# Kernel optimization log

Measured on AMD Instinct MI355X. Metric: run time of the kernel, lower is better.

The kernel has to match this reference:

```python
import jax, jax.numpy as jnp
import numpy as np

CUTOFFS = [2000, 10000, 50000]
HIDDEN = 1024
BATCH = 2048


def setup_inputs() -> dict:
    key = jax.random.key(0)
    ks = jax.random.split(key, 8)
    s = 1.0 / np.sqrt(HIDDEN)
    return {
        "hidden": jax.random.normal(ks[0], (BATCH, HIDDEN), dtype=jnp.float32),
        "target": jax.random.randint(ks[1], (BATCH,), 0, CUTOFFS[-1]),
        # head weight: candidates[:cutoffs[0]] plus 2 tail vectors, transposed -> (hidden, 2002)
        "head_w": jax.random.normal(ks[2], (HIDDEN, CUTOFFS[0] + 2), dtype=jnp.float32) * s,
        # tail 0 (cluster [2000,10000), size 8000): down 1024->1024 (rf^0), decode 1024->8000
        "down0": jax.random.normal(ks[3], (HIDDEN, HIDDEN), dtype=jnp.float32) * s,
        "dec0": jax.random.normal(ks[4], (HIDDEN, CUTOFFS[1] - CUTOFFS[0]), dtype=jnp.float32) * s,
        # tail 1 (cluster [10000,50000), size 40000): down 1024->256 (rf^1), decode 256->40000
        "down1": jax.random.normal(ks[5], (HIDDEN, HIDDEN // 4), dtype=jnp.float32) * s,
        "dec1": jax.random.normal(ks[6], (HIDDEN // 4, CUTOFFS[2] - CUTOFFS[1]), dtype=jnp.float32) * s,
    }


def reference(hidden, target, head_w, down0, dec0, down1, dec1):
    # Head logits over first bucket + one pseudo-token per tail cluster.
    head = hidden @ head_w  # (B, 2002)
    # Cluster membership masks (fixed shapes instead of data-dependent gather;
    # rows outside a cluster produce zeroed logits, matching index_select semantics
    # up to padding).
    m0 = ((target >= CUTOFFS[0]) & (target < CUTOFFS[1])).astype(hidden.dtype)
    m1 = ((target >= CUTOFFS[1]) & (target < CUTOFFS[2])).astype(hidden.dtype)
    # Grouped small matmuls: down-project then decode per tail cluster.
    t0 = ((hidden @ down0) @ dec0) * m0[:, None]  # (B, 8000)
    t1 = ((hidden @ down1) @ dec1) * m1[:, None]  # (B, 40000)
    return jnp.concatenate([head, t0, t1], axis=1)  # (B, 50002)
```

## Files before the change

kernel.cpp:

```cpp
#include <hip/hip_runtime.h>

typedef unsigned short u16;
typedef unsigned int   u32;
typedef __attribute__((ext_vector_type(4))) float  f32x4;
typedef __attribute__((ext_vector_type(8))) __bf16 bf16x8;
typedef __attribute__((ext_vector_type(8))) u16    u16x8;
typedef __attribute__((address_space(1))) void as1_void;
typedef __attribute__((address_space(3))) void as3_void;

__device__ int g_idx0[2048];
__device__ int g_idx1[2048];
__device__ int g_cnt[2];

__device__ __forceinline__ void async16(const void* g, void* l) {
  __builtin_amdgcn_global_load_lds((const as1_void*)g, (as3_void*)l, 16, 0, 0);
}

__device__ __forceinline__ u16 f2bf(float f) {
  u32 u = __builtin_bit_cast(u32, f);
  return (u16)((u + 0x7fffu + ((u >> 16) & 1u)) >> 16);
}

template <int MODE>
__device__ __forceinline__ void gemm_core(
    u16* As, u16* Bs,
    const u16* __restrict__ A, const u16* __restrict__ Bt,
    void* __restrict__ Cout, int K, int ldc, int colOff, int Nreal,
    const int* __restrict__ idx, int cnt, int bm, int bn)
{
  const int tid  = threadIdx.x;
  const int wid  = tid >> 6;
  const int lane = tid & 63;
  const int quad = lane >> 4;
  const int l16  = lane & 15;
  const int wm = (wid >> 1) * 64;
  const int wn = (wid & 1) * 64;

  f32x4 acc[4][4] = {};

  const int srow = wid * 16 + (lane >> 2);
  const int scol = (lane & 3) * 8;

  size_t ar0, ar1;
  if (MODE == 1) { ar0 = (size_t)idx[bm + srow]; ar1 = (size_t)idx[bm + srow + 64]; }
  else           { ar0 = (size_t)(bm + srow);    ar1 = ar0 + 64; }
  const u16* ga0 = A + ar0 * K + scol;
  const u16* ga1 = A + ar1 * K + scol;
  const u16* gb0 = Bt + (size_t)(bn + srow) * K + scol;
  const u16* gb1 = gb0 + (size_t)64 * K;

  for (int k0 = 0; k0 < K; k0 += 32) {
    async16(ga0 + k0, As + wid * 512);
    async16(ga1 + k0, As + wid * 512 + 2048);
    async16(gb0 + k0, Bs + wid * 512);
    async16(gb1 + k0, Bs + wid * 512 + 2048);
    __syncthreads();

    bf16x8 af[4], bfr[4];
#pragma unroll
    for (int i = 0; i < 4; i++) {
      af[i]  = *reinterpret_cast<const bf16x8*>(As + (wm + i * 16 + l16) * 32 + quad * 8);
      bfr[i] = *reinterpret_cast<const bf16x8*>(Bs + (wn + i * 16 + l16) * 32 + quad * 8);
    }
#pragma unroll
    for (int mi = 0; mi < 4; mi++)
#pragma unroll
      for (int ni = 0; ni < 4; ni++)
        acc[mi][ni] = __builtin_amdgcn_mfma_f32_16x16x32_bf16(af[mi], bfr[ni], acc[mi][ni], 0, 0, 0);
    __syncthreads();
  }

#pragma unroll
  for (int mi = 0; mi < 4; mi++) {
    const int rbase = bm + wm + mi * 16 + quad * 4;
    int  orow[4];
    bool vld[4];
#pragma unroll
    for (int r = 0; r < 4; r++) {
      if (MODE == 2) {
        int slot = rbase + r;
        vld[r]  = slot < cnt;
        orow[r] = vld[r] ? idx[slot] : 0;
      } else {
        vld[r] = true; orow[r] = rbase + r;
      }
    }
#pragma unroll
    for (int ni = 0; ni < 4; ni++) {
      const int col = bn + wn + ni * 16 + l16;
      if (MODE == 1) {
        u16* C = (u16*)Cout;
#pragma unroll
        for (int r = 0; r < 4; r++)
          C[(size_t)orow[r] * ldc + col] = f2bf(acc[mi][ni][r]);
      } else {
        if (col < Nreal) {
          float* C = (float*)Cout;
#pragma unroll
          for (int r = 0; r < 4; r++)
            if (vld[r]) C[(size_t)orow[r] * ldc + colOff + col] = acc[mi][ni][r];
        }
      }
    }
  }
}

__device__ __forceinline__ void tconv_core(float (*tile)[33], const float* __restrict__ in,
                                           u16* __restrict__ out, int K, int N, int bx, int by) {
  int tx = threadIdx.x & 31, ty = threadIdx.x >> 5;
  int n0 = bx * 32, k0 = by * 32;
#pragma unroll
  for (int i = 0; i < 4; i++) {
    int k = k0 + ty + i * 8;
    int n = n0 + tx;
    tile[ty + i * 8][tx] = (n < N) ? in[(size_t)k * N + n] : 0.0f;
  }
  __syncthreads();
#pragma unroll
  for (int i = 0; i < 4; i++)
    out[(size_t)(n0 + ty + i * 8) * K + k0 + tx] = f2bf(tile[tx][ty + i * 8]);
}

__global__ __launch_bounds__(256) void prep(
    const float* __restrict__ hidden, const int* __restrict__ target,
    const float* __restrict__ head_w, const float* __restrict__ down0,
    const float* __restrict__ dec0, const float* __restrict__ down1,
    const float* __restrict__ dec1,
    u16* __restrict__ hA, u16* __restrict__ head_wT, u16* __restrict__ down0T,
    u16* __restrict__ dec0T, u16* __restrict__ down1T, u16* __restrict__ dec1T)
{
  __shared__ float tile[32][33];
  __shared__ int cc[2];
  const int b = blockIdx.x;
  const int tid = threadIdx.x;
  if (b < 1024) {
    int i = b * 256 + tid;
    const float4* p = reinterpret_cast<const float4*>(hidden) + (size_t)i * 2;
    float4 a = p[0], c = p[1];
    u16x8 o;
    o[0] = f2bf(a.x); o[1] = f2bf(a.y); o[2] = f2bf(a.z); o[3] = f2bf(a.w);
    o[4] = f2bf(c.x); o[5] = f2bf(c.y); o[6] = f2bf(c.z); o[7] = f2bf(c.w);
    reinterpret_cast<u16x8*>(hA)[i] = o;
  } else if (b < 3072) {
    int r = b - 1024;  tconv_core(tile, head_w, head_wT, 1024, 2002,  r % 64,   r / 64);
  } else if (b < 4096) {
    int r = b - 3072;  tconv_core(tile, down0,  down0T,  1024, 1024,  r % 32,   r / 32);
  } else if (b < 12160) {
    int r = b - 4096;  tconv_core(tile, dec0,   dec0T,   1024, 8000,  r % 252,  r / 252);
  } else if (b < 12416) {
    int r = b - 12160; tconv_core(tile, down1,  down1T,  1024, 256,   r % 8,    r / 8);
  } else if (b < 22432) {
    int r = b - 12416; tconv_core(tile, dec1,   dec1T,   256,  40000, r % 1252, r / 1252);
  } else {
    if (tid < 2) cc[tid] = 0;
    __syncthreads();
    for (int i = tid; i < 2048; i += 256) {
      int t = target[i];
      if (t >= 2000 && t < 10000)  g_idx0[atomicAdd(&cc[0], 1)] = i;
      else if (t >= 10000)         g_idx1[atomicAdd(&cc[1], 1)] = i;
    }
    __syncthreads();
    int n0 = cc[0], n1 = cc[1];
    for (int i = tid; i < 2048; i += 256) {
      if (i >= n0) g_idx0[i] = 0;
      if (i >= n1) g_idx1[i] = 0;
    }
    if (tid == 0) { g_cnt[0] = n0; g_cnt[1] = n1; }
  }
}

__global__ __launch_bounds__(256, 2) void g1(
    const u16* __restrict__ hA, const u16* __restrict__ head_wT,
    const u16* __restrict__ down0T, const u16* __restrict__ down1T,
    u16* __restrict__ X0c, u16* __restrict__ X1c, float* __restrict__ out)
{
  __shared__ u16 As[4096], Bs[4096];
  const int b = blockIdx.x;
  if (b < 256) {
    gemm_core<0>(As, Bs, hA, head_wT, out, 1024, 50002, 0, 2002,
                 nullptr, 2048, (b >> 4) * 128, (b & 15) * 128);
  } else if (b < 384) {
    int r = b - 256, bm = (r & 15) * 128, bn = (r >> 4) * 128;
    if (bm < g_cnt[0])
      gemm_core<1>(As, Bs, hA, down0T, X0c, 1024, 1024, 0, 1024, g_idx0, g_cnt[0], bm, bn);
  } else {
    int r = b - 384, bm = (r & 15) * 128, bn = (r >> 4) * 128;
    if (bm < g_cnt[1])
      gemm_core<1>(As, Bs, hA, down1T, X1c, 1024, 256, 0, 256, g_idx1, g_cnt[1], bm, bn);
  }
}

__global__ __launch_bounds__(256, 2) void g2(
    const u16* __restrict__ X0c, const u16* __restrict__ X1c,
    const u16* __restrict__ dec0T, const u16* __restrict__ dec1T,
    const int* __restrict__ target, float* __restrict__ out)
{
  __shared__ u16 As[4096], Bs[4096];
  const int b = blockIdx.x;
  if (b < 1008) {
    int bm = (b & 15) * 128, bn = (b >> 4) * 128;
    if (bm < g_cnt[0])
      gemm_core<2>(As, Bs, X0c, dec0T, out, 1024, 50002, 2002, 8000, g_idx0, g_cnt[0], bm, bn);
  } else if (b < 6016) {
    int r = b - 1008, bm = (r & 15) * 128, bn = (r >> 4) * 128;
    if (bm < g_cnt[1])
      gemm_core<2>(As, Bs, X1c, dec1T, out, 256, 50002, 10002, 40000, g_idx1, g_cnt[1], bm, bn);
  } else {
    int row = b - 6016;
    int t = target[row];
    bool in0 = (t >= 2000) && (t < 10000);
    bool in1 = (t >= 10000);
    float2* p = reinterpret_cast<float2*>(out + (size_t)row * 50002);
    float2 z; z.x = 0.0f; z.y = 0.0f;
    if (!in0)
      for (int i = threadIdx.x; i < 4000; i += 256)  p[1001 + i] = z;
    if (!in1)
      for (int i = threadIdx.x; i < 20000; i += 256) p[5001 + i] = z;
  }
}

extern "C" void kernel_launch(void* const* d_in, const int* in_sizes, int n_in,
                              void* d_out, int out_size, void* d_ws, size_t ws_size,
                              hipStream_t stream) {
  const float* hidden = (const float*)d_in[0];
  const int*   target = (const int*)d_in[1];
  const float* head_w = (const float*)d_in[2];
  const float* down0  = (const float*)d_in[3];
  const float* dec0   = (const float*)d_in[4];
  const float* down1  = (const float*)d_in[5];
  const float* dec1   = (const float*)d_in[6];
  float* out = (float*)d_out;

  char* ws = (char*)d_ws;
  const size_t NEED = 53280768;
  if (ws_size < NEED) return;
  u16* hA      = (u16*)(ws);
  u16* head_wT = (u16*)(ws + 4194304);
  u16* down0T  = (u16*)(ws + 8388608);
  u16* dec0T   = (u16*)(ws + 10485760);
  u16* down1T  = (u16*)(ws + 27000832);
  u16* dec1T   = (u16*)(ws + 27525120);
  u16* X0c     = (u16*)(ws + 48037888);
  u16* X1c     = (u16*)(ws + 52232192);

  prep<<<22433, 256, 0, stream>>>(hidden, target, head_w, down0, dec0, down1, dec1,
                                  hA, head_wT, down0T, dec0T, down1T, dec1T);
  g1<<<416, 256, 0, stream>>>(hA, head_wT, down0T, down1T, X0c, X1c, out);
  g2<<<8064, 256, 0, stream>>>(X0c, X1c, dec0T, dec1T, target, out);
}
```

Measured before the change: 603.9 us.

## Widen GEMM K-tile to 64 with XOR-swizzled LDS, vectorize transposes, remap blocks

The GEMM core now stages a 64-wide K slice per iteration. LDS chunks are XOR-swizzled to avoid bank conflicts, so there are half as many barrier round trips and more MFMA work per sync. The transpose writes are vectorized to 4-wide u16 stores. Zero-filling of non-member rows moves from the second GEMM kernel into the prep kernel, and block indices in both GEMM kernels are remapped across 8 groups, presumably to spread work across XCDs. LDS use per block doubles and the tail-zeroing now runs before the GEMMs instead of in parallel with them.

```diff
diff --git a/kernel.cpp b/kernel.cpp
--- a/kernel.cpp
+++ b/kernel.cpp
@@ -4,6 +4,7 @@
 typedef unsigned int   u32;
 typedef __attribute__((ext_vector_type(4))) float  f32x4;
 typedef __attribute__((ext_vector_type(8))) __bf16 bf16x8;
+typedef __attribute__((ext_vector_type(4))) u16    u16x4;
 typedef __attribute__((ext_vector_type(8))) u16    u16x8;
 typedef __attribute__((address_space(1))) void as1_void;
 typedef __attribute__((address_space(3))) void as3_void;
@@ -38,35 +39,41 @@
 
   f32x4 acc[4][4] = {};
 
-  const int srow = wid * 16 + (lane >> 2);
-  const int scol = (lane & 3) * 8;
-
-  size_t ar0, ar1;
-  if (MODE == 1) { ar0 = (size_t)idx[bm + srow]; ar1 = (size_t)idx[bm + srow + 64]; }
-  else           { ar0 = (size_t)(bm + srow);    ar1 = ar0 + 64; }
-  const u16* ga0 = A + ar0 * K + scol;
-  const u16* ga1 = A + ar1 * K + scol;
-  const u16* gb0 = Bt + (size_t)(bn + srow) * K + scol;
-  const u16* gb1 = gb0 + (size_t)64 * K;
-
-  for (int k0 = 0; k0 < K; k0 += 32) {
-    async16(ga0 + k0, As + wid * 512);
-    async16(ga1 + k0, As + wid * 512 + 2048);
-    async16(gb0 + k0, Bs + wid * 512);
-    async16(gb1 + k0, Bs + wid * 512 + 2048);
-    __syncthreads();
-
-    bf16x8 af[4], bfr[4];
-#pragma unroll
-    for (int i = 0; i < 4; i++) {
-      af[i]  = *reinterpret_cast<const bf16x8*>(As + (wm + i * 16 + l16) * 32 + quad * 8);
-      bfr[i] = *reinterpret_cast<const bf16x8*>(Bs + (wn + i * 16 + l16) * 32 + quad * 8);
-    }
-#pragma unroll
-    for (int mi = 0; mi < 4; mi++)
-#pragma unroll
-      for (int ni = 0; ni < 4; ni++)
-        acc[mi][ni] = __builtin_amdgcn_mfma_f32_16x16x32_bf16(af[mi], bfr[ni], acc[mi][ni], 0, 0, 0);
+  const int sr = lane >> 3;
+  const int sc = ((lane & 7) ^ sr) * 8;
+
+  const u16* pa[4];
+  const u16* pb[4];
+#pragma unroll
+  for (int j = 0; j < 4; j++) {
+    int r = wid * 32 + j * 8 + sr;
+    size_t ar = (MODE == 1) ? (size_t)idx[bm + r] : (size_t)(bm + r);
+    pa[j] = A  + ar * K + sc;
+    pb[j] = Bt + (size_t)(bn + r) * K + sc;
+  }
+
+  for (int k0 = 0; k0 < K; k0 += 64) {
+#pragma unroll
+    for (int j = 0; j < 4; j++) async16(pa[j] + k0, As + (wid * 32 + j * 8) * 64);
+#pragma unroll
+    for (int j = 0; j < 4; j++) async16(pb[j] + k0, Bs + (wid * 32 + j * 8) * 64);
+    __syncthreads();
+
+#pragma unroll
+    for (int ks = 0; ks < 2; ks++) {
+      bf16x8 af[4], bfr[4];
+#pragma unroll
+      for (int i = 0; i < 4; i++) {
+        const int chunk = ((ks * 4 + quad) ^ (l16 & 7)) * 8;
+        af[i]  = *reinterpret_cast<const bf16x8*>(As + (wm + i * 16 + l16) * 64 + chunk);
+        bfr[i] = *reinterpret_cast<const bf16x8*>(Bs + (wn + i * 16 + l16) * 64 + chunk);
+      }
+#pragma unroll
+      for (int mi = 0; mi < 4; mi++)
+#pragma unroll
+        for (int ni = 0; ni < 4; ni++)
+          acc[mi][ni] = __builtin_amdgcn_mfma_f32_16x16x32_bf16(af[mi], bfr[ni], acc[mi][ni], 0, 0, 0);
+    }
     __syncthreads();
   }
 
@@ -116,9 +123,12 @@
     tile[ty + i * 8][tx] = (n < N) ? in[(size_t)k * N + n] : 0.0f;
   }
   __syncthreads();
-#pragma unroll
-  for (int i = 0; i < 4; i++)
-    out[(size_t)(n0 + ty + i * 8) * K + k0 + tx] = f2bf(tile[tx][ty + i * 8]);
+  int n = threadIdx.x >> 3;
+  int kq = (threadIdx.x & 7) * 4;
+  u16x4 o;
+#pragma unroll
+  for (int j = 0; j < 4; j++) o[j] = f2bf(tile[kq + j][n]);
+  *reinterpret_cast<u16x4*>(out + (size_t)(n0 + n) * K + k0 + kq) = o;
 }
 
 __global__ __launch_bounds__(256) void prep(
@@ -127,7 +137,8 @@
     const float* __restrict__ dec0, const float* __restrict__ down1,
     const float* __restrict__ dec1,
     u16* __restrict__ hA, u16* __restrict__ head_wT, u16* __restrict__ down0T,
-    u16* __restrict__ dec0T, u16* __restrict__ down1T, u16* __restrict__ dec1T)
+    u16* __restrict__ dec0T, u16* __restrict__ down1T, u16* __restrict__ dec1T,
+    float* __restrict__ out)
 {
   __shared__ float tile[32][33];
   __shared__ int cc[2];
@@ -151,6 +162,17 @@
     int r = b - 12160; tconv_core(tile, down1,  down1T,  1024, 256,   r % 8,    r / 8);
   } else if (b < 22432) {
     int r = b - 12416; tconv_core(tile, dec1,   dec1T,   256,  40000, r % 1252, r / 1252);
+  } else if (b < 24480) {
+    int row = b - 22432;
+    int t = target[row];
+    bool in0 = (t >= 2000) && (t < 10000);
+    bool in1 = (t >= 10000);
+    float2* p = reinterpret_cast<float2*>(out + (size_t)row * 50002);
+    float2 z; z.x = 0.0f; z.y = 0.0f;
+    if (!in0)
+      for (int i = tid; i < 4000; i += 256)  p[1001 + i] = z;
+    if (!in1)
+      for (int i = tid; i < 20000; i += 256) p[5001 + i] = z;
   } else {
     if (tid < 2) cc[tid] = 0;
     __syncthreads();
@@ -169,13 +191,14 @@
   }
 }
 
-__global__ __launch_bounds__(256, 2) void g1(
+__global__ __launch_bounds__(256, 2) void gemmA(
     const u16* __restrict__ hA, const u16* __restrict__ head_wT,
     const u16* __restrict__ down0T, const u16* __restrict__ down1T,
     u16* __restrict__ X0c, u16* __restrict__ X1c, float* __restrict__ out)
 {
-  __shared__ u16 As[4096], Bs[4096];
-  const int b = blockIdx.x;
+  __shared__ alignas(16) u16 As[128 * 64];
+  __shared__ alignas(16) u16 Bs[128 * 64];
+  const int b = (blockIdx.x & 7) * 52 + (blockIdx.x >> 3);
   if (b < 256) {
     gemm_core<0>(As, Bs, hA, head_wT, out, 1024, 50002, 0, 2002,
                  nullptr, 2048, (b >> 4) * 128, (b & 15) * 128);
@@ -190,32 +213,22 @@
   }
 }
 
-__global__ __launch_bounds__(256, 2) void g2(
+__global__ __launch_bounds__(256, 2) void gemmB(
     const u16* __restrict__ X0c, const u16* __restrict__ X1c,
     const u16* __restrict__ dec0T, const u16* __restrict__ dec1T,
-    const int* __restrict__ target, float* __restrict__ out)
-{
-  __shared__ u16 As[4096], Bs[4096];
-  const int b = blockIdx.x;
+    float* __restrict__ out)
+{
+  __shared__ alignas(16) u16 As[128 * 64];
+  __shared__ alignas(16) u16 Bs[128 * 64];
+  const int b = (blockIdx.x & 7) * 752 + (blockIdx.x >> 3);
   if (b < 1008) {
     int bm = (b & 15) * 128, bn = (b >> 4) * 128;
     if (bm < g_cnt[0])
       gemm_core<2>(As, Bs, X0c, dec0T, out, 1024, 50002, 2002, 8000, g_idx0, g_cnt[0], bm, bn);
-  } else if (b < 6016) {
+  } else {
     int r = b - 1008, bm = (r & 15) * 128, bn = (r >> 4) * 128;
     if (bm < g_cnt[1])
       gemm_core<2>(As, Bs, X1c, dec1T, out, 256, 50002, 10002, 40000, g_idx1, g_cnt[1], bm, bn);
-  } else {
-    int row = b - 6016;
-    int t = target[row];
-    bool in0 = (t >= 2000) && (t < 10000);
-    bool in1 = (t >= 10000);
-    float2* p = reinterpret_cast<float2*>(out + (size_t)row * 50002);
-    float2 z; z.x = 0.0f; z.y = 0.0f;
-    if (!in0)
-      for (int i = threadIdx.x; i < 4000; i += 256)  p[1001 + i] = z;
-    if (!in1)
-      for (int i = threadIdx.x; i < 20000; i += 256) p[5001 + i] = z;
   }
 }
 
@@ -243,8 +256,8 @@
   u16* X0c     = (u16*)(ws + 48037888);
   u16* X1c     = (u16*)(ws + 52232192);
 
-  prep<<<22433, 256, 0, stream>>>(hidden, target, head_w, down0, dec0, down1, dec1,
-                                  hA, head_wT, down0T, dec0T, down1T, dec1T);
-  g1<<<416, 256, 0, stream>>>(hA, head_wT, down0T, down1T, X0c, X1c, out);
-  g2<<<8064, 256, 0, stream>>>(X0c, X1c, dec0T, dec1T, target, out);
-}
+  prep<<<24481, 256, 0, stream>>>(hidden, target, head_w, down0, dec0, down1, dec1,
+                                  hA, head_wT, down0T, dec0T, down1T, dec1T, out);
+  gemmA<<<416, 256, 0, stream>>>(hA, head_wT, down0T, down1T, X0c, X1c, out);
+  gemmB<<<6016, 256, 0, stream>>>(X0c, X1c, dec0T, dec1T, out);
+}
```

Result: no change. 604.3 us (+0.1%).
